# Optimization experiments

Measured on AMD Instinct MI355X. Metric: run time of the kernel, lower is better.

The kernel has to match this reference:

```python
import jax, jax.numpy as jnp
import numpy as np

HEADS = 20


def cape_embed(f, P):
    # f: [b, s, d], P: [b, s, 4, 4]; rotate channel groups of 4 by P
    b, s, d = f.shape
    f4 = f.reshape(b, s, d // 4, 4)
    out = jnp.einsum('bsik,bskj->bsij', f4, P)
    return out.reshape(b, s, d)


def setup_inputs() -> dict:
    key = jax.random.key(0)
    ks = jax.random.split(key, 9)
    bt, l, d = 2, 1024, 1280  # (b*t_out, tokens, channels)
    t_out, b = 2, 1
    sd = 1.0 / np.sqrt(d)
    return {
        'hidden_states': jax.random.normal(ks[0], (bt, l, d), jnp.float32),
        'p_out': jax.random.normal(ks[1], (b, t_out, 4, 4), jnp.float32) * 0.5,
        'p_out_inv': jax.random.normal(ks[2], (b, t_out, 4, 4), jnp.float32) * 0.5,
        'Wq': jax.random.normal(ks[3], (d, d), jnp.float32) * sd,
        'Wk': jax.random.normal(ks[4], (d, d), jnp.float32) * sd,
        'Wv': jax.random.normal(ks[5], (d, d), jnp.float32) * sd,
        'Wo': jax.random.normal(ks[6], (d, d), jnp.float32) * sd,
        'bo': jnp.zeros((d,), jnp.float32),
    }


def reference(hidden_states, p_out, p_out_inv, Wq, Wk, Wv, Wo, bo):
    residual = hidden_states  # [(b t_out), l, d]
    b = p_out.shape[0]
    t_out = p_out.shape[1]
    bt, l, d = hidden_states.shape
    s = t_out * l
    hd = d // HEADS
    scale = hd ** -0.5

    # rearrange '(b t_out) l d -> b (t_out l) d'
    hs = hidden_states.reshape(b, s, d)

    q = hs @ Wq
    k = hs @ Wk
    v = hs @ Wv

    # repeat per-frame CAPE matrices over spatial tokens: 'b t f g -> b (t l) f g'
    Pq = jnp.repeat(p_out_inv, l, axis=1)  # [b, s, 4, 4]
    Pk = jnp.repeat(p_out, l, axis=1)      # self-attn: p_in := p_out
    q = cape_embed(q, Pq)
    k = cape_embed(k, Pk)

    # head split: [b, s, d] -> [b, h, s, hd]
    qh = q.reshape(b, s, HEADS, hd).transpose(0, 2, 1, 3)
    kh = k.reshape(b, s, HEADS, hd).transpose(0, 2, 1, 3)
    vh = v.reshape(b, s, HEADS, hd).transpose(0, 2, 1, 3)

    scores = jnp.einsum('bhsd,bhtd->bhst', qh, kh) * scale
    probs = jax.nn.softmax(scores, axis=-1)
    out = jnp.einsum('bhst,bhtd->bhsd', probs, vh)

    out = out.transpose(0, 2, 1, 3).reshape(b, s, d)
    out = out @ Wo + bo

    # rearrange 'b (t_out l) d -> (b t_out) l d'
    out = out.reshape(bt, l, d)
    out = out + residual  # residual_connection; rescale_output_factor = 1.0
    return out
```

## Files before the change

### kernel.cpp

```cpp
#include <hip/hip_runtime.h>

typedef short short8 __attribute__((ext_vector_type(8)));
typedef short short4v __attribute__((ext_vector_type(4)));
typedef float f32x4 __attribute__((ext_vector_type(4)));
typedef float float4v __attribute__((ext_vector_type(4)));
typedef __bf16 bf16x8 __attribute__((ext_vector_type(8)));
typedef _Float16 half4 __attribute__((ext_vector_type(4)));
typedef _Float16 half2v __attribute__((ext_vector_type(2)));

__device__ __forceinline__ short f2bf(float x) {
  unsigned u = __builtin_bit_cast(unsigned, x);
  u += 0x7fffu + ((u >> 16) & 1u);
  return (short)(u >> 16);
}

__device__ __forceinline__ f32x4 mfma16(short8 a, short8 b, f32x4 c) {
  return __builtin_amdgcn_mfma_f32_16x16x32_bf16(
      __builtin_bit_cast(bf16x8, a), __builtin_bit_cast(bf16x8, b), c, 0, 0, 0);
}

__device__ __forceinline__ void async16(void* lds, const void* g) {
  __builtin_amdgcn_global_load_lds(
      (const __attribute__((address_space(1))) unsigned*)g,
      (__attribute__((address_space(3))) unsigned*)lds, 16, 0, 0);
}


__global__ __launch_bounds__(256) void cvt_bf16_kernel(
    const float* __restrict__ x, short* __restrict__ y, int n4) {
  int i = blockIdx.x * 256 + threadIdx.x;
  if (i < n4) {
    float4v v = *(const float4v*)(x + (size_t)i * 4);
    short4v o;
#pragma unroll
    for (int j = 0; j < 4; j++) o[j] = f2bf(v[j]);
    *(short4v*)(y + (size_t)i * 4) = o;
  }
}

__global__ __launch_bounds__(256) void capeT_all_kernel(
    const float* __restrict__ Wq, const float* __restrict__ Wk,
    const float* __restrict__ Wv, const float* __restrict__ Wo,
    const float* __restrict__ p_inv, const float* __restrict__ p_out,
    float qscale, short* __restrict__ BT0, short* __restrict__ BT1,
    short* __restrict__ wo_t) {
  const int ND = 1280, KD = 1280;
  const size_t SEC = (size_t)1280 * 1280;
  int z = blockIdx.z;
  const float* W;
  const float* P;
  float scale = 1.0f;
  short *d0, *d1;
  if (z == 0) { W = Wq; P = p_inv; scale = qscale; d0 = BT0; d1 = BT1; }
  else if (z == 1) { W = Wk; P = p_out; d0 = BT0 + SEC; d1 = BT1 + SEC; }
  else if (z == 2) { W = Wv; P = nullptr; d0 = BT0 + 2 * SEC; d1 = BT1 + 2 * SEC; }
  else { W = Wo; P = nullptr; d0 = wo_t; d1 = nullptr; }

  __shared__ float tile[32][33];
  int bn = blockIdx.x * 32, bk = blockIdx.y * 32;
  int tx = threadIdx.x, ty = threadIdx.y;
  for (int i = ty; i < 32; i += 8)
    tile[i][tx] = W[(size_t)(bk + i) * ND + bn + tx];
  __syncthreads();
  for (int c = ty; c < 32; c += 8) {
    float v0, v1;
    if (P) {
      int g = c & ~3, jj = c & 3;
      float a0 = 0.f, a1 = 0.f;
#pragma unroll
      for (int j = 0; j < 4; j++) {
        float wv = tile[tx][g + j];
        a0 += wv * P[j * 4 + jj];
        a1 += wv * P[16 + j * 4 + jj];
      }
      v0 = a0 * scale;
      v1 = a1 * scale;
    } else {
      v0 = v1 = tile[tx][c] * scale;
    }
    size_t o = (size_t)(bn + c) * KD + bk + tx;
    d0[o] = f2bf(v0);
    if (d1) d1[o] = f2bf(v1);
  }
}


__global__ __launch_bounds__(256) void gemm128_qkv_kernel(
    const short* __restrict__ A, const short* __restrict__ B0,
    const short* __restrict__ B1, int M, int N, int K,
    short* __restrict__ qb, short* __restrict__ ktl,
    _Float16* __restrict__ vtl) {
  __shared__ __align__(16) short As[2][128][32];
  __shared__ __align__(16) short Bs[2][128][32];
  int tid = threadIdx.x;
  int l = tid & 63, w = tid >> 6;
  int wr = w >> 1, wc = w & 1;
  int lr = l & 15, lg = l >> 4;
  int bm = blockIdx.y * 128, bn = blockIdx.x * 128;
  const short* BT = (bm >= 1024) ? B1 : B0;
  f32x4 acc[4][4] = {};

  auto stage = [&](int b, int k0) {
    const short* ga = A + (size_t)(bm + (tid >> 2)) * K + k0 + (tid & 3) * 8;
    const short* gb = BT + (size_t)(bn + (tid >> 2)) * K + k0 + (tid & 3) * 8;
    char* la = (char*)&As[b][0][0] + w * 1024;
    char* lb = (char*)&Bs[b][0][0] + w * 1024;
    async16(la, ga);
    async16(la + 4096, ga + (size_t)64 * K);
    async16(lb, gb);
    async16(lb + 4096, gb + (size_t)64 * K);
  };

  auto compute = [&](int b) {
    const short* Ab = &As[b][0][0];
    const short* Bb = &Bs[b][0][0];
    short8 af[4], bf_[4];
#pragma unroll
    for (int mi = 0; mi < 4; mi++)
      af[mi] = *(const short8*)(Ab + (wr * 64 + mi * 16 + lr) * 32 + lg * 8);
#pragma unroll
    for (int nj = 0; nj < 4; nj++)
      bf_[nj] = *(const short8*)(Bb + (wc * 64 + nj * 16 + lr) * 32 + lg * 8);
#pragma unroll
    for (int mi = 0; mi < 4; mi++)
#pragma unroll
      for (int nj = 0; nj < 4; nj++)
        acc[mi][nj] = mfma16(af[mi], bf_[nj], acc[mi][nj]);
  };

  int nk = K >> 5;
  stage(0, 0);
  for (int ks = 0; ks < nk; ks += 2) {
    __syncthreads();
    if (ks + 1 < nk) stage(1, (ks + 1) << 5);
    compute(0);
    __syncthreads();
    if (ks + 2 < nk) stage(0, (ks + 2) << 5);
    compute(1);
  }

#pragma unroll
  for (int mi = 0; mi < 4; mi++)
#pragma unroll
    for (int nj = 0; nj < 4; nj++)
#pragma unroll
      for (int i = 0; i < 4; i++) {
        int row = bm + wr * 64 + mi * 16 + lg * 4 + i;
        int col = bn + wc * 64 + nj * 16 + lr;
        float v = acc[mi][nj][i];
        int s = row;
        if (col < 1280) {
          qb[(((size_t)(col >> 6)) * 2048 + s) * 64 + (col & 63)] = f2bf(v);
        } else if (col < 2560) {
          int cc = col - 1280;
          int h = cc >> 6, d = cc & 63;
          int kt = s >> 6, r = s & 63;
          int kcol = (((d >> 3) ^ (r & 7)) << 3) | (d & 7);
          ktl[(((size_t)h * 32 + kt) * 64 + r) * 64 + kcol] = f2bf(v);
        } else {
          int cc = col - 2560;
          int h = cc >> 6, dv = cc & 63;
          int kt = s >> 6, kk = s & 63;
          int vcol = (((kk >> 2) ^ (dv & 15)) << 2) | (kk & 3);
          vtl[(((size_t)h * 32 + kt) * 64 + dv) * 64 + vcol] = (_Float16)v;
        }
      }
}


__global__ __launch_bounds__(256) void gemm64_o_kernel(
    const short* __restrict__ A, const short* __restrict__ BT,
    int M, int N, int K, const float* __restrict__ bias,
    const float* __restrict__ resid, float* __restrict__ out) {
  __shared__ __align__(16) short As[2][64][32];
  __shared__ __align__(16) short Bs[2][64][32];
  int tid = threadIdx.x;
  int l = tid & 63, w = tid >> 6;
  int wr = w >> 1, wc = w & 1;
  int lr = l & 15, lg = l >> 4;
  int bm = blockIdx.y * 64, bn = blockIdx.x * 64;
  f32x4 acc[2][2] = {};

  auto stage = [&](int b, int k0) {
    const short* ga = A + (size_t)(bm + (tid >> 2)) * K + k0 + (tid & 3) * 8;
    const short* gb = BT + (size_t)(bn + (tid >> 2)) * K + k0 + (tid & 3) * 8;
    async16((char*)&As[b][0][0] + w * 1024, ga);
    async16((char*)&Bs[b][0][0] + w * 1024, gb);
  };

  auto compute = [&](int b) {
    const short* Ab = &As[b][0][0];
    const short* Bb = &Bs[b][0][0];
    short8 af[2], bf_[2];
#pragma unroll
    for (int mi = 0; mi < 2; mi++)
      af[mi] = *(const short8*)(Ab + (wr * 32 + mi * 16 + lr) * 32 + lg * 8);
#pragma unroll
    for (int nj = 0; nj < 2; nj++)
      bf_[nj] = *(const short8*)(Bb + (wc * 32 + nj * 16 + lr) * 32 + lg * 8);
#pragma unroll
    for (int mi = 0; mi < 2; mi++)
#pragma unroll
      for (int nj = 0; nj < 2; nj++)
        acc[mi][nj] = mfma16(af[mi], bf_[nj], acc[mi][nj]);
  };

  int nk = K >> 5;
  stage(0, 0);
  for (int ks = 0; ks < nk; ks += 2) {
    __syncthreads();
    if (ks + 1 < nk) stage(1, (ks + 1) << 5);
    compute(0);
    __syncthreads();
    if (ks + 2 < nk) stage(0, (ks + 2) << 5);
    compute(1);
  }

#pragma unroll
  for (int mi = 0; mi < 2; mi++)
#pragma unroll
    for (int nj = 0; nj < 2; nj++)
#pragma unroll
      for (int i = 0; i < 4; i++) {
        int row = bm + wr * 32 + mi * 16 + lg * 4 + i;
        int col = bn + wc * 32 + nj * 16 + lr;
        out[(size_t)row * N + col] =
            acc[mi][nj][i] + bias[col] + resid[(size_t)row * N + col];
      }
}

__global__ __launch_bounds__(256) void attn_kernel(
    const short* __restrict__ qb, const short* __restrict__ k_tiled,
    const _Float16* __restrict__ v_tiled, short* __restrict__ attn_out) {
  const int S = 2048, HD = 64;
  int h = blockIdx.x;
  int qblk = blockIdx.y;
  int tid = threadIdx.x;
  int w = tid >> 6, l = tid & 63;
  int lr = l & 15, lg = l >> 4;
  int q0 = qblk * 64 + w * 16;

  __shared__ __align__(16) short Kl[2][64][64];
  __shared__ __align__(16) _Float16 Vl[2][64][64];

  const short* qptr = qb + ((size_t)h * S + q0 + lr) * HD;
  short8 qf0 = *(const short8*)(qptr + lg * 8);
  short8 qf1 = *(const short8*)(qptr + 32 + lg * 8);

  auto stageKV = [&](int b, int kt) {
    const short* gk = k_tiled + (((size_t)h * 32 + kt) << 12) + tid * 8;
    const _Float16* gv = v_tiled + (((size_t)h * 32 + kt) << 12) + tid * 8;
    char* lk = (char*)&Kl[b][0][0] + w * 1024;
    char* lv = (char*)&Vl[b][0][0] + w * 1024;
    async16(lk, gk);
    async16(lk + 4096, gk + 2048);
    async16(lv, gv);
    async16(lv + 4096, gv + 2048);
  };

  float m = -1e30f, lsum = 0.f;
  f32x4 oacc[4] = {};

  auto compute_tile = [&](int buf) {
    const short* Kb = &Kl[buf][0][0];
    const _Float16* Vb = &Vl[buf][0][0];
    f32x4 st[4];
    __builtin_amdgcn_s_setprio(1);
#pragma unroll
    for (int kk = 0; kk < 4; kk++) {
      int r = kk * 16 + lr;
      int sw = r & 7;
      short8 kf0 = *(const short8*)(Kb + r * 64 + ((lg ^ sw) << 3));
      short8 kf1 = *(const short8*)(Kb + r * 64 + (((4 + lg) ^ sw) << 3));
      f32x4 s0 = {};
      s0 = mfma16(kf0, qf0, s0);
      s0 = mfma16(kf1, qf1, s0);
      st[kk] = s0;
    }
    __builtin_amdgcn_s_setprio(0);
    float m0 = fmaxf(fmaxf(st[0][0], st[0][1]), fmaxf(st[0][2], st[0][3]));
    float m1 = fmaxf(fmaxf(st[1][0], st[1][1]), fmaxf(st[1][2], st[1][3]));
    float m2 = fmaxf(fmaxf(st[2][0], st[2][1]), fmaxf(st[2][2], st[2][3]));
    float m3 = fmaxf(fmaxf(st[3][0], st[3][1]), fmaxf(st[3][2], st[3][3]));
    float tm = fmaxf(fmaxf(m0, m1), fmaxf(m2, m3));
    tm = fmaxf(tm, __shfl_xor(tm, 16));
    tm = fmaxf(tm, __shfl_xor(tm, 32));
    if (!__all(tm <= m + 8.0f)) {
      float mnew = fmaxf(m, tm);
      float fac = __builtin_amdgcn_exp2f(m - mnew);
      lsum *= fac;
#pragma unroll
      for (int i = 0; i < 4; i++) {
        float fi = __shfl(fac, lg * 4 + i);
#pragma unroll
        for (int nb = 0; nb < 4; nb++) oacc[nb][i] *= fi;
      }
      m = mnew;
    }
    half4 pf[4];
    float ps[4];
#pragma unroll
    for (int kk = 0; kk < 4; kk++) {
      float p0 = __builtin_amdgcn_exp2f(st[kk][0] - m);
      float p1 = __builtin_amdgcn_exp2f(st[kk][1] - m);
      float p2 = __builtin_amdgcn_exp2f(st[kk][2] - m);
      float p3 = __builtin_amdgcn_exp2f(st[kk][3] - m);
      half2v lo = __builtin_bit_cast(half2v, __builtin_amdgcn_cvt_pkrtz(p0, p1));
      half2v hi = __builtin_bit_cast(half2v, __builtin_amdgcn_cvt_pkrtz(p2, p3));
      pf[kk][0] = lo[0]; pf[kk][1] = lo[1];
      pf[kk][2] = hi[0]; pf[kk][3] = hi[1];
      ps[kk] = (p0 + p1) + (p2 + p3);
    }
    lsum += (ps[0] + ps[1]) + (ps[2] + ps[3]);
#pragma unroll
    for (int kk = 0; kk < 4; kk++) {
      half4 vf[4];
#pragma unroll
      for (int nb = 0; nb < 4; nb++) {
        int dv = nb * 16 + lr;
        vf[nb] = *(const half4*)(Vb + dv * 64 + ((((kk << 2) + lg) ^ lr) << 2));
      }
      __builtin_amdgcn_s_setprio(1);
#pragma unroll
      for (int nb = 0; nb < 4; nb++)
        oacc[nb] = __builtin_amdgcn_mfma_f32_16x16x16f16(pf[kk], vf[nb], oacc[nb], 0, 0, 0);
      __builtin_amdgcn_s_setprio(0);
    }
  };

  stageKV(0, 0);
  for (int kt2 = 0; kt2 < 32; kt2 += 2) {
    __syncthreads();
    if (kt2 + 1 < 32) stageKV(1, kt2 + 1);
    compute_tile(0);
    __syncthreads();
    if (kt2 + 2 < 32) stageKV(0, kt2 + 2);
    compute_tile(1);
  }

  lsum += __shfl_xor(lsum, 16);
  lsum += __shfl_xor(lsum, 32);

#pragma unroll
  for (int i = 0; i < 4; i++) {
    float li = __shfl(lsum, lg * 4 + i);
    float inv = 1.0f / li;
    int row = q0 + lg * 4 + i;
#pragma unroll
    for (int nb = 0; nb < 4; nb++)
      attn_out[(size_t)row * 1280 + h * 64 + nb * 16 + lr] = f2bf(oacc[nb][i] * inv);
  }
}


extern "C" void kernel_launch(void* const* d_in, const int* in_sizes, int n_in,
                              void* d_out, int out_size, void* d_ws, size_t ws_size,
                              hipStream_t stream) {
  const float* hs = (const float*)d_in[0];
  const float* p_out = (const float*)d_in[1];
  const float* p_inv = (const float*)d_in[2];
  const float* Wq = (const float*)d_in[3];
  const float* Wk = (const float*)d_in[4];
  const float* Wv = (const float*)d_in[5];
  const float* Wo = (const float*)d_in[6];
  const float* bo = (const float*)d_in[7];
  float* out = (float*)d_out;
  char* ws = (char*)d_ws;

  short* hs_bf = (short*)(ws + 0);
  short* BT0 = (short*)(ws + 5242880);
  short* BT1 = (short*)(ws + 15073280);
  short* wo_t = (short*)(ws + 24903680);
  short* q_bf = (short*)(ws + 28180480);
  short* k_tiled = (short*)(ws + 33423360);
  _Float16* v_tiled = (_Float16*)(ws + 38666240);
  short* attn_bf = (short*)(ws + 43909120);

  const float QSCALE = 0.125f * 1.44269504f;
  const int n4 = 2048 * 1280 / 4;
  cvt_bf16_kernel<<<(n4 + 255) / 256, 256, 0, stream>>>(hs, hs_bf, n4);

  capeT_all_kernel<<<dim3(40, 40, 4), dim3(32, 8), 0, stream>>>(
      Wq, Wk, Wv, Wo, p_inv, p_out, QSCALE, BT0, BT1, wo_t);

  gemm128_qkv_kernel<<<dim3(30, 16), 256, 0, stream>>>(
      hs_bf, BT0, BT1, 2048, 3840, 1280, q_bf, k_tiled, v_tiled);

  attn_kernel<<<dim3(20, 32), 256, 0, stream>>>(q_bf, k_tiled, v_tiled, attn_bf);

  gemm64_o_kernel<<<dim3(20, 32), 256, 0, stream>>>(
      attn_bf, wo_t, 2048, 1280, 1280, bo, hs, out);
}
```

Baseline: 124.9 us.

## Triple-buffer attention KV staging, merge bf16 cast into prep kernel

The attention kernel moves from a two-slot K/V LDS double buffer with two barriers per pair of tiles to a three-slot ring. It uses explicit vmcnt waits and one barrier per tile, so loads run two tiles ahead. The running-max check now tests the per-lane partial max first and only does the cross-lane shuffles when a rescale is needed. Separately, the hidden-state fp32-to-bf16 conversion becomes an extra z-slice of the weight-prep kernel, removing one launch. These changes cost more LDS per block, which may lower occupancy, and depend on the hand-written vmcnt count being correct.

```diff
diff --git a/kernel.cpp b/kernel.cpp
--- a/kernel.cpp
+++ b/kernel.cpp
@@ -25,28 +25,34 @@
       (__attribute__((address_space(3))) unsigned*)lds, 16, 0, 0);
 }
 
-
-__global__ __launch_bounds__(256) void cvt_bf16_kernel(
-    const float* __restrict__ x, short* __restrict__ y, int n4) {
-  int i = blockIdx.x * 256 + threadIdx.x;
-  if (i < n4) {
-    float4v v = *(const float4v*)(x + (size_t)i * 4);
-    short4v o;
-#pragma unroll
-    for (int j = 0; j < 4; j++) o[j] = f2bf(v[j]);
-    *(short4v*)(y + (size_t)i * 4) = o;
-  }
-}
-
 __global__ __launch_bounds__(256) void capeT_all_kernel(
     const float* __restrict__ Wq, const float* __restrict__ Wk,
     const float* __restrict__ Wv, const float* __restrict__ Wo,
     const float* __restrict__ p_inv, const float* __restrict__ p_out,
     float qscale, short* __restrict__ BT0, short* __restrict__ BT1,
-    short* __restrict__ wo_t) {
+    short* __restrict__ wo_t, const float* __restrict__ hs,
+    short* __restrict__ hs_bf) {
   const int ND = 1280, KD = 1280;
   const size_t SEC = (size_t)1280 * 1280;
   int z = blockIdx.z;
+  int tx = threadIdx.x, ty = threadIdx.y;
+  if (z == 4) {
+    int t = ty * 32 + tx;
+    int base = ((blockIdx.y * 40 + blockIdx.x) * 256 + t) * 2;
+    const int n4 = 2048 * 1280 / 4;
+#pragma unroll
+    for (int r = 0; r < 2; r++) {
+      int i = base + r;
+      if (i < n4) {
+        float4v v = *(const float4v*)(hs + (size_t)i * 4);
+        short4v o;
+#pragma unroll
+        for (int j = 0; j < 4; j++) o[j] = f2bf(v[j]);
+        *(short4v*)(hs_bf + (size_t)i * 4) = o;
+      }
+    }
+    return;
+  }
   const float* W;
   const float* P;
   float scale = 1.0f;
@@ -58,7 +64,6 @@
 
   __shared__ float tile[32][33];
   int bn = blockIdx.x * 32, bk = blockIdx.y * 32;
-  int tx = threadIdx.x, ty = threadIdx.y;
   for (int i = ty; i < 32; i += 8)
     tile[i][tx] = W[(size_t)(bk + i) * ND + bn + tx];
   __syncthreads();
@@ -240,8 +245,8 @@
   int lr = l & 15, lg = l >> 4;
   int q0 = qblk * 64 + w * 16;
 
-  __shared__ __align__(16) short Kl[2][64][64];
-  __shared__ __align__(16) _Float16 Vl[2][64][64];
+  __shared__ __align__(16) short Kl[3][64][64];
+  __shared__ __align__(16) _Float16 Vl[3][64][64];
 
   const short* qptr = qb + ((size_t)h * S + q0 + lr) * HD;
   short8 qf0 = *(const short8*)(qptr + lg * 8);
@@ -282,10 +287,11 @@
     float m1 = fmaxf(fmaxf(st[1][0], st[1][1]), fmaxf(st[1][2], st[1][3]));
     float m2 = fmaxf(fmaxf(st[2][0], st[2][1]), fmaxf(st[2][2], st[2][3]));
     float m3 = fmaxf(fmaxf(st[3][0], st[3][1]), fmaxf(st[3][2], st[3][3]));
-    float tm = fmaxf(fmaxf(m0, m1), fmaxf(m2, m3));
-    tm = fmaxf(tm, __shfl_xor(tm, 16));
-    tm = fmaxf(tm, __shfl_xor(tm, 32));
-    if (!__all(tm <= m + 8.0f)) {
+    float pmax = fmaxf(fmaxf(m0, m1), fmaxf(m2, m3));
+    if (!__all(pmax <= m + 8.0f)) {
+      float tm = pmax;
+      tm = fmaxf(tm, __shfl_xor(tm, 16));
+      tm = fmaxf(tm, __shfl_xor(tm, 32));
       float mnew = fmaxf(m, tm);
       float fac = __builtin_amdgcn_exp2f(m - mnew);
       lsum *= fac;
@@ -329,13 +335,18 @@
   };
 
   stageKV(0, 0);
-  for (int kt2 = 0; kt2 < 32; kt2 += 2) {
-    __syncthreads();
-    if (kt2 + 1 < 32) stageKV(1, kt2 + 1);
-    compute_tile(0);
-    __syncthreads();
-    if (kt2 + 2 < 32) stageKV(0, kt2 + 2);
-    compute_tile(1);
+  stageKV(1, 1);
+  for (int t = 0; t < 32; ++t) {
+    if (t < 31) {
+      asm volatile("s_waitcnt vmcnt(4)" ::: "memory");
+    } else {
+      asm volatile("s_waitcnt vmcnt(0)" ::: "memory");
+    }
+    __builtin_amdgcn_sched_barrier(0);
+    __builtin_amdgcn_s_barrier();
+    __builtin_amdgcn_sched_barrier(0);
+    if (t + 2 < 32) stageKV((t + 2) % 3, t + 2);
+    compute_tile(t % 3);
   }
 
   lsum += __shfl_xor(lsum, 16);
@@ -377,11 +388,9 @@
   short* attn_bf = (short*)(ws + 43909120);
 
   const float QSCALE = 0.125f * 1.44269504f;
-  const int n4 = 2048 * 1280 / 4;
-  cvt_bf16_kernel<<<(n4 + 255) / 256, 256, 0, stream>>>(hs, hs_bf, n4);
-
-  capeT_all_kernel<<<dim3(40, 40, 4), dim3(32, 8), 0, stream>>>(
-      Wq, Wk, Wv, Wo, p_inv, p_out, QSCALE, BT0, BT1, wo_t);
+
+  capeT_all_kernel<<<dim3(40, 40, 5), dim3(32, 8), 0, stream>>>(
+      Wq, Wk, Wv, Wo, p_inv, p_out, QSCALE, BT0, BT1, wo_t, hs, hs_bf);
 
   gemm128_qkv_kernel<<<dim3(30, 16), 256, 0, stream>>>(
       hs_bf, BT0, BT1, 2048, 3840, 1280, q_bf, k_tiled, v_tiled);
```

Measured after the change: 121.5 us. 1.03x faster.
